# Kernel optimization log

Measured on AMD Instinct MI355X. Metric: run time of the kernel, lower is better.

## Reference

```python
import jax, jax.numpy as jnp
import numpy as np

HEADS = 8
KV_HEADS = 4
HEAD_DIM = 256
HIDDEN = 2560
WINDOW = 1024          # sliding_window (layer is sliding: (0+1) % 6 != 0)
SCALE = 256.0 ** -0.5  # query_pre_attn_scalar ** -0.5
ROPE_BASE = 10000.0    # rope_local_base_freq for sliding layers
EPS = 1e-6
NEG = -1e30


def rms_norm(x, w, eps=EPS):
    # x: [..., D]; effective weight is (1 + param) per the RMSNorm module
    var = jnp.mean(x * x, axis=-1, keepdims=True)
    return x * jax.lax.rsqrt(var + eps) * w


def rope(x, base, offset):
    # x: [B, H, T, D]; rotate-half RoPE over the full head_dim
    T, D = x.shape[2], x.shape[3]
    half = D // 2
    pos = (offset + jnp.arange(T)).astype(jnp.float32)           # [T]
    inv_freq = base ** (-jnp.arange(half, dtype=jnp.float32) * 2.0 / D)  # [half]
    ang = pos[:, None] * inv_freq[None, :]                       # [T, half]
    cos, sin = jnp.cos(ang), jnp.sin(ang)
    x1, x2 = x[..., :half], x[..., half:]
    return jnp.concatenate([x1 * cos - x2 * sin, x2 * cos + x1 * sin], axis=-1)


def setup_inputs() -> dict:
    key = jax.random.key(0)
    ks = jax.random.split(key, 7)
    B, T, S = 2, 1024, 4096
    w_std = 0.02
    return {
        "x": jax.random.normal(ks[0], (B, T, HIDDEN), dtype=jnp.float32),
        "k_cache": jax.random.normal(ks[1], (B, KV_HEADS, S, HEAD_DIM), dtype=jnp.float32),
        "v_cache": jax.random.normal(ks[2], (B, KV_HEADS, S, HEAD_DIM), dtype=jnp.float32),
        "wq": jax.random.normal(ks[3], (HIDDEN, HEADS * HEAD_DIM), dtype=jnp.float32) * w_std,
        "wk": jax.random.normal(ks[4], (HIDDEN, KV_HEADS * HEAD_DIM), dtype=jnp.float32) * w_std,
        "wv": jax.random.normal(ks[5], (HIDDEN, KV_HEADS * HEAD_DIM), dtype=jnp.float32) * w_std,
        "wo": jax.random.normal(ks[6], (HEADS * HEAD_DIM, HIDDEN), dtype=jnp.float32) * w_std,
        "q_norm_w": jnp.zeros((HEAD_DIM,), dtype=jnp.float32),
        "k_norm_w": jnp.zeros((HEAD_DIM,), dtype=jnp.float32),
        "pos_offset": 2048,
        "cache_index": 2048,
    }


def reference(x, k_cache, v_cache, wq, wk, wv, wo, q_norm_w, k_norm_w, pos_offset, cache_index):
    B, T, _ = x.shape
    # QKV projections -> [B, H, T, D]
    q = (x @ wq).reshape(B, T, HEADS, HEAD_DIM).transpose(0, 2, 1, 3)
    k = (x @ wk).reshape(B, T, KV_HEADS, HEAD_DIM).transpose(0, 2, 1, 3)
    v = (x @ wv).reshape(B, T, KV_HEADS, HEAD_DIM).transpose(0, 2, 1, 3)
    # per-head RMSNorm (effective weight 1 + param)
    q = rms_norm(q, 1.0 + q_norm_w)
    k = rms_norm(k, 1.0 + k_norm_w)
    # RoPE with position offset
    q = rope(q, ROPE_BASE, pos_offset)
    k = rope(k, ROPE_BASE, pos_offset)
    # KV cache update at cache_index along the sequence axis
    k_new = jax.lax.dynamic_update_slice(k_cache, k, (0, 0, cache_index, 0))
    v_new = jax.lax.dynamic_update_slice(v_cache, v, (0, 0, cache_index, 0))
    S = k_new.shape[2]
    # sliding-window validity mask over cached keys (as in the module: shared over queries)
    idx = jnp.arange(S)
    valid = (idx < cache_index + T) & (idx >= cache_index + T - WINDOW)   # [S]
    # GQA attention: group queries over kv heads
    G = HEADS // KV_HEADS
    qg = q.reshape(B, KV_HEADS, G, T, HEAD_DIM)
    scores = jnp.einsum('bkgtd,bksd->bkgts', qg, k_new) * SCALE           # [B,KV,G,T,S]
    scores = jnp.where(valid[None, None, None, None, :], scores, NEG)
    p = jax.nn.softmax(scores, axis=-1)
    out = jnp.einsum('bkgts,bksd->bkgtd', p, v_new)                       # [B,KV,G,T,D]
    out = out.reshape(B, HEADS, T, HEAD_DIM).transpose(0, 2, 1, 3).reshape(B, T, HEADS * HEAD_DIM)
    return out @ wo, k_new, v_new
```

## Files before the change

kernel.cpp:

```cpp
#include <hip/hip_runtime.h>

typedef __bf16 bf16;
typedef __bf16 bf16x8 __attribute__((ext_vector_type(8)));
typedef __bf16 bf16x4 __attribute__((ext_vector_type(4)));
typedef float f32x4 __attribute__((ext_vector_type(4)));

#define MFMA16(a, b, c) __builtin_amdgcn_mfma_f32_16x16x32_bf16(a, b, c, 0, 0, 0)

#define GLL(lds, g)                                                    \
  __builtin_amdgcn_global_load_lds(                                    \
      (const __attribute__((address_space(1))) void*)(g),              \
      (__attribute__((address_space(3))) void*)(lds), 16, 0, 0)

__global__ __launch_bounds__(256) void cache_copy_kernel(
    const float* __restrict__ kc, const float* __restrict__ vc,
    float* __restrict__ kout, float* __restrict__ vout,
    const int* __restrict__ p_ci) {
  const int s = blockIdx.x * 4 + (threadIdx.x >> 6);
  const int bk = blockIdx.y;
  const int ci = *p_ci;
  if ((unsigned)(s - ci) < 1024u) return;
  const long base = ((long)bk * 4096 + s) * 64 + (threadIdx.x & 63);
  ((float4*)kout)[base] = ((const float4*)kc)[base];
  ((float4*)vout)[base] = ((const float4*)vc)[base];
}

__global__ __launch_bounds__(256) void cvt_x_kernel(const float* __restrict__ x,
                                                    bf16* __restrict__ xb) {
  const long i = (long)blockIdx.x * 256 + threadIdx.x;
  const float4 v = ((const float4*)x)[i];
  bf16x4 o4;
  o4.x = (bf16)v.x; o4.y = (bf16)v.y; o4.z = (bf16)v.z; o4.w = (bf16)v.w;
  ((bf16x4*)xb)[i] = o4;
}

__global__ __launch_bounds__(256) void wqkv_trans_kernel(const float* __restrict__ wq,
                                                         const float* __restrict__ wk,
                                                         const float* __restrict__ wv,
                                                         bf16* __restrict__ dst) {
  __shared__ float tile[32][33];
  const int k0 = blockIdx.x * 32, n0 = blockIdx.y * 32;
  const float* src; int col, srcN;
  if (n0 < 2048)      { src = wq; col = n0;        srcN = 2048; }
  else if (n0 < 3072) { src = wk; col = n0 - 2048; srcN = 1024; }
  else                { src = wv; col = n0 - 3072; srcN = 1024; }
  const int tx = threadIdx.x, ty = threadIdx.y;
#pragma unroll
  for (int i = 0; i < 4; ++i)
    tile[ty + i * 8][tx] = src[(long)(k0 + ty + i * 8) * srcN + col + tx];
  __syncthreads();
#pragma unroll
  for (int i = 0; i < 4; ++i)
    dst[(long)(n0 + ty + i * 8) * 2560 + k0 + tx] = (bf16)tile[tx][ty + i * 8];
}

__global__ __launch_bounds__(256) void wo_trans_kernel(const float* __restrict__ wo,
                                                       bf16* __restrict__ dst) {
  __shared__ float tile[32][33];
  const int k0 = blockIdx.x * 32, n0 = blockIdx.y * 32;
  const int tx = threadIdx.x, ty = threadIdx.y;
#pragma unroll
  for (int i = 0; i < 4; ++i)
    tile[ty + i * 8][tx] = wo[(long)(k0 + ty + i * 8) * 2560 + n0 + tx];
  __syncthreads();
#pragma unroll
  for (int i = 0; i < 4; ++i)
    dst[(long)(n0 + ty + i * 8) * 2048 + k0 + tx] = (bf16)tile[tx][ty + i * 8];
}

__global__ __launch_bounds__(256) void v_trans_kernel(const float* __restrict__ vout,
                                                      const int* __restrict__ p_ci,
                                                      bf16* __restrict__ vt) {
  __shared__ float tile[32][33];
  const int s0 = blockIdx.x * 32, d0 = blockIdx.y * 32, bk = blockIdx.z;
  const int ci = *p_ci;
  const int tx = threadIdx.x, ty = threadIdx.y;
  const float* src = vout + ((long)bk * 4096 + ci) * 256;
#pragma unroll
  for (int i = 0; i < 4; ++i)
    tile[ty + i * 8][tx] = src[(long)(s0 + ty + i * 8) * 256 + d0 + tx];
  __syncthreads();
  bf16* dstb = vt + ((long)bk * 256 + d0) * 1024 + s0;
#pragma unroll
  for (int i = 0; i < 4; ++i)
    dstb[(long)(ty + i * 8) * 1024 + tx] = (bf16)tile[tx][ty + i * 8];
}

template <int K, int N>
__global__ __launch_bounds__(256) void gemm_kernel(const bf16* __restrict__ A,
                                                   const bf16* __restrict__ BT,
                                                   float* __restrict__ C) {
  __shared__ bf16 As[128 * 64];
  __shared__ bf16 Bs[64 * 64];
  const int bm = blockIdx.x, bn = blockIdx.y;
  const int tid = threadIdx.x;
  const int wave = tid >> 6, lane = tid & 63;
  const int quad = lane >> 4, l16 = lane & 15;
  const int wm = (wave & 1) * 64, wn = (wave >> 1) * 32;
  f32x4 acc[4][2] = {};
  const int srow = tid >> 3;
  const int scol = tid & 7;
  const bf16* Ag = A + (long)(bm * 128) * K;
  const bf16* Bg = BT + (long)(bn * 64) * K;
  for (int k0 = 0; k0 < K; k0 += 64) {
    __syncthreads();
#pragma unroll
    for (int i = 0; i < 4; ++i) {
      const int r = i * 32 + srow;
      GLL(As + (i * 256 + wave * 64) * 8, Ag + (long)r * K + k0 + (scol ^ (r & 7)) * 8);
    }
#pragma unroll
    for (int i = 0; i < 2; ++i) {
      const int r = i * 32 + srow;
      GLL(Bs + (i * 256 + wave * 64) * 8, Bg + (long)r * K + k0 + (scol ^ (r & 7)) * 8);
    }
    __syncthreads();
#pragma unroll
    for (int kk = 0; kk < 2; ++kk) {
      bf16x8 af[4], bfr[2];
#pragma unroll
      for (int mi = 0; mi < 4; ++mi) {
        const int r = wm + mi * 16 + l16;
        af[mi] = *(const bf16x8*)(As + r * 64 + (((kk * 4 + quad) ^ (r & 7)) * 8));
      }
#pragma unroll
      for (int ni = 0; ni < 2; ++ni) {
        const int r = wn + ni * 16 + l16;
        bfr[ni] = *(const bf16x8*)(Bs + r * 64 + (((kk * 4 + quad) ^ (r & 7)) * 8));
      }
#pragma unroll
      for (int mi = 0; mi < 4; ++mi)
#pragma unroll
        for (int ni = 0; ni < 2; ++ni)
          acc[mi][ni] = MFMA16(af[mi], bfr[ni], acc[mi][ni]);
    }
  }
  const int crow = bm * 128 + wm + quad * 4;
  const int ccol = bn * 64 + wn + l16;
#pragma unroll
  for (int mi = 0; mi < 4; ++mi)
#pragma unroll
    for (int ni = 0; ni < 2; ++ni)
#pragma unroll
      for (int r = 0; r < 4; ++r)
        C[(long)(crow + mi * 16 + r) * N + ccol + ni * 16] = acc[mi][ni][r];
}

__global__ __launch_bounds__(256) void normrope_kernel(
    const float* __restrict__ qkv, const float* __restrict__ qw,
    const float* __restrict__ kw, const int* __restrict__ p_pos,
    const int* __restrict__ p_ci, float* __restrict__ kout,
    float* __restrict__ vout, bf16* __restrict__ q_bf, bf16* __restrict__ k_bf) {
  const int bt = blockIdx.x, slot = blockIdx.y;
  const int t = bt & 1023, b = bt >> 10;
  const int d = threadIdx.x;
  const float val = qkv[(long)bt * 4096 + slot * 256 + d];
  const int ci = *p_ci;
  if (slot >= 12) {
    vout[((long)(b * 4 + (slot - 12)) * 4096 + ci + t) * 256 + d] = val;
    return;
  }
  __shared__ float red[4];
  __shared__ float rowbuf[256];
  float ss = val * val;
#pragma unroll
  for (int i = 1; i < 64; i <<= 1) ss += __shfl_xor(ss, i);
  if ((d & 63) == 0) red[d >> 6] = ss;
  __syncthreads();
  const float tot = red[0] + red[1] + red[2] + red[3];
  const float rstd = rsqrtf(tot * (1.0f / 256.0f) + 1e-6f);
  const bool isq = slot < 8;
  const float wv = isq ? qw[d] : kw[d];
  const float nv = val * rstd * (1.0f + wv);
  rowbuf[d] = nv;
  __syncthreads();
  const int e = d & 127;
  const float inv_freq = exp2f((float)e * -0.10381025296522976f);
  const float ang = (float)(*p_pos + t) * inv_freq;
  float sn, cs;
  sincosf(ang, &sn, &cs);
  float outv;
  if (d < 128) outv = nv * cs - rowbuf[d + 128] * sn;
  else         outv = nv * cs + rowbuf[d - 128] * sn;
  if (isq) {
    q_bf[((long)(b * 8 + slot) * 1024 + t) * 256 + d] = (bf16)outv;
  } else {
    const int kh = slot - 8;
    kout[((long)(b * 4 + kh) * 4096 + ci + t) * 256 + d] = outv;
    k_bf[((long)(b * 4 + kh) * 1024 + t) * 256 + d] = (bf16)outv;
  }
}

__global__ __launch_bounds__(256) void attn_kernel(const bf16* __restrict__ q_bf,
                                                   const bf16* __restrict__ k_bf,
                                                   const bf16* __restrict__ vt_bf,
                                                   bf16* __restrict__ attn) {
  __shared__ bf16 Ks[64 * 256];
  __shared__ bf16 Vs[256 * 64];
  __shared__ bf16 Ps[64 * 72];
  const int qt = blockIdx.x, h = blockIdx.y, b = blockIdx.z;
  const int kvh = h >> 1;
  const int tid = threadIdx.x;
  const int wave = tid >> 6, lane = tid & 63, quad = lane >> 4, l16 = lane & 15;
  bf16x8 qf[8];
  const bf16* qg =
      q_bf + ((long)(b * 8 + h) * 1024 + qt * 64 + wave * 16 + l16) * 256 + quad * 8;
#pragma unroll
  for (int i = 0; i < 8; ++i) qf[i] = *(const bf16x8*)(qg + i * 32);
  f32x4 o[16] = {};
  float m_r[4] = {-1e30f, -1e30f, -1e30f, -1e30f};
  float l_r[4] = {0.f, 0.f, 0.f, 0.f};
  const float sfac = 0.0625f * 1.44269504088896f;
  const bf16* kgb = k_bf + (long)(b * 4 + kvh) * 1024 * 256;
  const bf16* vgb = vt_bf + (long)(b * 4 + kvh) * 256 * 1024;
  const int krow = tid >> 5, kccp = tid & 31;
  const int kcc = kccp ^ (krow & 7);
  const int vrow0 = tid >> 3, vccp = tid & 7;
  for (int st = 0; st < 16; ++st) {
    __syncthreads();
#pragma unroll
    for (int i = 0; i < 8; ++i) {
      GLL(Ks + (i * 256 + wave * 64) * 8,
          kgb + (long)(st * 64 + krow + i * 8) * 256 + kcc * 8);
    }
#pragma unroll
    for (int i = 0; i < 8; ++i) {
      const int vr = vrow0 + i * 32;
      GLL(Vs + (i * 256 + wave * 64) * 8,
          vgb + (long)vr * 1024 + st * 64 + (vccp ^ (vr & 7)) * 8);
    }
    __syncthreads();
    f32x4 sacc[4] = {};
#pragma unroll
    for (int kk = 0; kk < 8; ++kk) {
#pragma unroll
      for (int ni = 0; ni < 4; ++ni) {
        const int r = ni * 16 + l16;
        bf16x8 kf = *(const bf16x8*)(Ks + r * 256 + (((kk * 4 + quad) ^ (r & 7)) * 8));
        sacc[ni] = MFMA16(qf[kk], kf, sacc[ni]);
      }
    }
    float alpha_r[4];
#pragma unroll
    for (int r = 0; r < 4; ++r) {
      float s0 = sacc[0][r] * sfac, s1 = sacc[1][r] * sfac;
      float s2 = sacc[2][r] * sfac, s3 = sacc[3][r] * sfac;
      float mx = fmaxf(fmaxf(s0, s1), fmaxf(s2, s3));
#pragma unroll
      for (int dd = 1; dd < 16; dd <<= 1) mx = fmaxf(mx, __shfl_xor(mx, dd));
      float mnew = fmaxf(m_r[r], mx);
      float al = exp2f(m_r[r] - mnew);
      m_r[r] = mnew;
      alpha_r[r] = al;
      float p0 = exp2f(s0 - mnew), p1 = exp2f(s1 - mnew);
      float p2 = exp2f(s2 - mnew), p3 = exp2f(s3 - mnew);
      float rs = p0 + p1 + p2 + p3;
#pragma unroll
      for (int dd = 1; dd < 16; dd <<= 1) rs += __shfl_xor(rs, dd);
      l_r[r] = l_r[r] * al + rs;
      const int prow = (wave * 16 + quad * 4 + r) * 72;
      Ps[prow + l16] = (bf16)p0;
      Ps[prow + 16 + l16] = (bf16)p1;
      Ps[prow + 32 + l16] = (bf16)p2;
      Ps[prow + 48 + l16] = (bf16)p3;
    }
#pragma unroll
    for (int n2 = 0; n2 < 16; ++n2) {
      f32x4 tv = o[n2];
      tv.x *= alpha_r[0]; tv.y *= alpha_r[1]; tv.z *= alpha_r[2]; tv.w *= alpha_r[3];
      o[n2] = tv;
    }
    __syncthreads();
    bf16x8 pf0 = *(const bf16x8*)(Ps + (wave * 16 + l16) * 72 + quad * 8);
    bf16x8 pf1 = *(const bf16x8*)(Ps + (wave * 16 + l16) * 72 + 32 + quad * 8);
#pragma unroll
    for (int n2 = 0; n2 < 16; ++n2) {
      const int r = n2 * 16 + l16;
      bf16x8 vf0 = *(const bf16x8*)(Vs + r * 64 + ((quad ^ (r & 7)) * 8));
      o[n2] = MFMA16(pf0, vf0, o[n2]);
      bf16x8 vf1 = *(const bf16x8*)(Vs + r * 64 + (((4 + quad) ^ (r & 7)) * 8));
      o[n2] = MFMA16(pf1, vf1, o[n2]);
    }
  }
  float inv_l[4];
#pragma unroll
  for (int r = 0; r < 4; ++r) inv_l[r] = 1.0f / l_r[r];
  bf16* og = attn + ((long)(b * 1024 + qt * 64 + wave * 16 + quad * 4)) * 2048 +
             h * 256 + l16;
#pragma unroll
  for (int n2 = 0; n2 < 16; ++n2)
#pragma unroll
    for (int r = 0; r < 4; ++r)
      og[(long)r * 2048 + n2 * 16] = (bf16)(o[n2][r] * inv_l[r]);
}

extern "C" void kernel_launch(void* const* d_in, const int* in_sizes, int n_in,
                              void* d_out, int out_size, void* d_ws, size_t ws_size,
                              hipStream_t stream) {
  const float* x = (const float*)d_in[0];
  const float* k_cache = (const float*)d_in[1];
  const float* v_cache = (const float*)d_in[2];
  const float* wq = (const float*)d_in[3];
  const float* wk = (const float*)d_in[4];
  const float* wv = (const float*)d_in[5];
  const float* wo = (const float*)d_in[6];
  const float* qnw = (const float*)d_in[7];
  const float* knw = (const float*)d_in[8];
  const int* p_pos = (const int*)d_in[9];
  const int* p_ci = (const int*)d_in[10];

  float* out0 = (float*)d_out;
  float* kout = out0 + (long)2 * 1024 * 2560;
  float* vout = kout + (long)2 * 4 * 4096 * 256;

  char* w = (char*)d_ws;
  bf16* x_bf = (bf16*)(w);
  bf16* wqkv_t = (bf16*)(w + 10485760);
  bf16* wo_t = (bf16*)(w + 31457280);
  float* qkv = (float*)(w + 41943040);
  bf16* q_bf = (bf16*)(w + 75497472);
  bf16* k_bf = (bf16*)(w + 83886080);
  bf16* vt_bf = (bf16*)(w + 88080384);
  bf16* attn_b = (bf16*)(w + 92274688);

  cache_copy_kernel<<<dim3(1024, 8), 256, 0, stream>>>(k_cache, v_cache, kout,
                                                       vout, p_ci);

  cvt_x_kernel<<<5120, 256, 0, stream>>>(x, x_bf);
  dim3 tb(32, 8);
  wqkv_trans_kernel<<<dim3(80, 128), tb, 0, stream>>>(wq, wk, wv, wqkv_t);
  wo_trans_kernel<<<dim3(64, 80), tb, 0, stream>>>(wo, wo_t);

  gemm_kernel<2560, 4096><<<dim3(16, 64), 256, 0, stream>>>(x_bf, wqkv_t, qkv);

  normrope_kernel<<<dim3(2048, 16), 256, 0, stream>>>(qkv, qnw, knw, p_pos, p_ci,
                                                      kout, vout, q_bf, k_bf);

  v_trans_kernel<<<dim3(32, 8, 8), tb, 0, stream>>>(vout, p_ci, vt_bf);

  attn_kernel<<<dim3(16, 8, 2), 256, 0, stream>>>(q_bf, k_bf, vt_bf, attn_b);

  gemm_kernel<2048, 2560><<<dim3(16, 40), 256, 0, stream>>>(attn_b, wo_t, out0);
}
```

Baseline: 395.5 us.

## Merge prep kernels, double-buffer GEMM, bf16 QKV intermediate, retune tiles

Four preprocessing kernels (cache copy, x conversion, two weight transposes) are merged into one launch that dispatches on block index. The GEMM is templated on tile sizes and now double-buffers LDS with a K-step of 32, so the next tile's global-to-LDS load overlaps the current MFMA work. The QKV projection writes a bf16 intermediate instead of fp32, which halves that traffic. Tile shapes change for both GEMMs. The bf16 intermediate adds rounding before the RMS norm and also flows into the stored V cache values.

Result: no change. 398.8 us (+0.9%).

```diff
diff --git a/kernel.cpp b/kernel.cpp
--- a/kernel.cpp
+++ b/kernel.cpp
@@ -12,60 +12,63 @@
       (const __attribute__((address_space(1))) void*)(g),              \
       (__attribute__((address_space(3))) void*)(lds), 16, 0, 0)
 
-__global__ __launch_bounds__(256) void cache_copy_kernel(
+__global__ __launch_bounds__(256) void prep_kernel(
     const float* __restrict__ kc, const float* __restrict__ vc,
     float* __restrict__ kout, float* __restrict__ vout,
-    const int* __restrict__ p_ci) {
-  const int s = blockIdx.x * 4 + (threadIdx.x >> 6);
-  const int bk = blockIdx.y;
-  const int ci = *p_ci;
-  if ((unsigned)(s - ci) < 1024u) return;
-  const long base = ((long)bk * 4096 + s) * 64 + (threadIdx.x & 63);
-  ((float4*)kout)[base] = ((const float4*)kc)[base];
-  ((float4*)vout)[base] = ((const float4*)vc)[base];
-}
-
-__global__ __launch_bounds__(256) void cvt_x_kernel(const float* __restrict__ x,
-                                                    bf16* __restrict__ xb) {
-  const long i = (long)blockIdx.x * 256 + threadIdx.x;
-  const float4 v = ((const float4*)x)[i];
-  bf16x4 o4;
-  o4.x = (bf16)v.x; o4.y = (bf16)v.y; o4.z = (bf16)v.z; o4.w = (bf16)v.w;
-  ((bf16x4*)xb)[i] = o4;
-}
-
-__global__ __launch_bounds__(256) void wqkv_trans_kernel(const float* __restrict__ wq,
-                                                         const float* __restrict__ wk,
-                                                         const float* __restrict__ wv,
-                                                         bf16* __restrict__ dst) {
+    const int* __restrict__ p_ci, const float* __restrict__ x,
+    bf16* __restrict__ xb, const float* __restrict__ wq,
+    const float* __restrict__ wk, const float* __restrict__ wv,
+    bf16* __restrict__ wqkv_t, const float* __restrict__ wo,
+    bf16* __restrict__ wo_t) {
+  const int blk = blockIdx.x;
+  const int tid = threadIdx.x;
+  if (blk < 8192) {
+    const int s = (blk & 1023) * 4 + (tid >> 6);
+    const int bk = blk >> 10;
+    const int ci = *p_ci;
+    if ((unsigned)(s - ci) < 1024u) return;
+    const long base = ((long)bk * 4096 + s) * 64 + (tid & 63);
+    ((float4*)kout)[base] = ((const float4*)kc)[base];
+    ((float4*)vout)[base] = ((const float4*)vc)[base];
+    return;
+  }
+  if (blk < 13312) {
+    const long i = (long)(blk - 8192) * 256 + tid;
+    const float4 v = ((const float4*)x)[i];
+    bf16x4 o4;
+    o4.x = (bf16)v.x; o4.y = (bf16)v.y; o4.z = (bf16)v.z; o4.w = (bf16)v.w;
+    ((bf16x4*)xb)[i] = o4;
+    return;
+  }
   __shared__ float tile[32][33];
-  const int k0 = blockIdx.x * 32, n0 = blockIdx.y * 32;
-  const float* src; int col, srcN;
-  if (n0 < 2048)      { src = wq; col = n0;        srcN = 2048; }
-  else if (n0 < 3072) { src = wk; col = n0 - 2048; srcN = 1024; }
-  else                { src = wv; col = n0 - 3072; srcN = 1024; }
-  const int tx = threadIdx.x, ty = threadIdx.y;
-#pragma unroll
-  for (int i = 0; i < 4; ++i)
-    tile[ty + i * 8][tx] = src[(long)(k0 + ty + i * 8) * srcN + col + tx];
-  __syncthreads();
-#pragma unroll
-  for (int i = 0; i < 4; ++i)
-    dst[(long)(n0 + ty + i * 8) * 2560 + k0 + tx] = (bf16)tile[tx][ty + i * 8];
-}
-
-__global__ __launch_bounds__(256) void wo_trans_kernel(const float* __restrict__ wo,
-                                                       bf16* __restrict__ dst) {
-  __shared__ float tile[32][33];
-  const int k0 = blockIdx.x * 32, n0 = blockIdx.y * 32;
-  const int tx = threadIdx.x, ty = threadIdx.y;
-#pragma unroll
-  for (int i = 0; i < 4; ++i)
-    tile[ty + i * 8][tx] = wo[(long)(k0 + ty + i * 8) * 2560 + n0 + tx];
-  __syncthreads();
-#pragma unroll
-  for (int i = 0; i < 4; ++i)
-    dst[(long)(n0 + ty + i * 8) * 2048 + k0 + tx] = (bf16)tile[tx][ty + i * 8];
+  const int tx = tid & 31, ty = tid >> 5;
+  if (blk < 23552) {
+    const int idx = blk - 13312;
+    const int k0 = (idx % 80) * 32, n0 = (idx / 80) * 32;
+    const float* src; int col, srcN;
+    if (n0 < 2048)      { src = wq; col = n0;        srcN = 2048; }
+    else if (n0 < 3072) { src = wk; col = n0 - 2048; srcN = 1024; }
+    else                { src = wv; col = n0 - 3072; srcN = 1024; }
+#pragma unroll
+    for (int i = 0; i < 4; ++i)
+      tile[ty + i * 8][tx] = src[(long)(k0 + ty + i * 8) * srcN + col + tx];
+    __syncthreads();
+#pragma unroll
+    for (int i = 0; i < 4; ++i)
+      wqkv_t[(long)(n0 + ty + i * 8) * 2560 + k0 + tx] = (bf16)tile[tx][ty + i * 8];
+    return;
+  }
+  {
+    const int idx = blk - 23552;
+    const int k0 = (idx & 63) * 32, n0 = (idx >> 6) * 32;
+#pragma unroll
+    for (int i = 0; i < 4; ++i)
+      tile[ty + i * 8][tx] = wo[(long)(k0 + ty + i * 8) * 2560 + n0 + tx];
+    __syncthreads();
+#pragma unroll
+    for (int i = 0; i < 4; ++i)
+      wo_t[(long)(n0 + ty + i * 8) * 2048 + k0 + tx] = (bf16)tile[tx][ty + i * 8];
+  }
 }
 
 __global__ __launch_bounds__(256) void v_trans_kernel(const float* __restrict__ vout,
@@ -86,75 +89,85 @@
     dstb[(long)(ty + i * 8) * 1024 + tx] = (bf16)tile[tx][ty + i * 8];
 }
 
-template <int K, int N>
+template <int BM, int BN, int K, int N, typename OutT>
 __global__ __launch_bounds__(256) void gemm_kernel(const bf16* __restrict__ A,
                                                    const bf16* __restrict__ BT,
-                                                   float* __restrict__ C) {
-  __shared__ bf16 As[128 * 64];
-  __shared__ bf16 Bs[64 * 64];
+                                                   OutT* __restrict__ C) {
+  __shared__ bf16 As[2 * BM * 32];
+  __shared__ bf16 Bs[2 * BN * 32];
   const int bm = blockIdx.x, bn = blockIdx.y;
   const int tid = threadIdx.x;
   const int wave = tid >> 6, lane = tid & 63;
   const int quad = lane >> 4, l16 = lane & 15;
-  const int wm = (wave & 1) * 64, wn = (wave >> 1) * 32;
-  f32x4 acc[4][2] = {};
-  const int srow = tid >> 3;
-  const int scol = tid & 7;
-  const bf16* Ag = A + (long)(bm * 128) * K;
-  const bf16* Bg = BT + (long)(bn * 64) * K;
-  for (int k0 = 0; k0 < K; k0 += 64) {
-    __syncthreads();
-#pragma unroll
-    for (int i = 0; i < 4; ++i) {
-      const int r = i * 32 + srow;
-      GLL(As + (i * 256 + wave * 64) * 8, Ag + (long)r * K + k0 + (scol ^ (r & 7)) * 8);
-    }
-#pragma unroll
-    for (int i = 0; i < 2; ++i) {
-      const int r = i * 32 + srow;
-      GLL(Bs + (i * 256 + wave * 64) * 8, Bg + (long)r * K + k0 + (scol ^ (r & 7)) * 8);
-    }
-    __syncthreads();
-#pragma unroll
-    for (int kk = 0; kk < 2; ++kk) {
-      bf16x8 af[4], bfr[2];
-#pragma unroll
-      for (int mi = 0; mi < 4; ++mi) {
-        const int r = wm + mi * 16 + l16;
-        af[mi] = *(const bf16x8*)(As + r * 64 + (((kk * 4 + quad) ^ (r & 7)) * 8));
-      }
-#pragma unroll
-      for (int ni = 0; ni < 2; ++ni) {
-        const int r = wn + ni * 16 + l16;
-        bfr[ni] = *(const bf16x8*)(Bs + r * 64 + (((kk * 4 + quad) ^ (r & 7)) * 8));
-      }
-#pragma unroll
-      for (int mi = 0; mi < 4; ++mi)
-#pragma unroll
-        for (int ni = 0; ni < 2; ++ni)
-          acc[mi][ni] = MFMA16(af[mi], bfr[ni], acc[mi][ni]);
-    }
-  }
-  const int crow = bm * 128 + wm + quad * 4;
-  const int ccol = bn * 64 + wn + l16;
-#pragma unroll
-  for (int mi = 0; mi < 4; ++mi)
-#pragma unroll
-    for (int ni = 0; ni < 2; ++ni)
+  constexpr int WM = BM / 2, WN = BN / 2;
+  constexpr int MI = WM / 16, NI = WN / 16;
+  const int wm = (wave & 1) * WM, wn = (wave >> 1) * WN;
+  f32x4 acc[MI][NI] = {};
+  const int srow = tid >> 2;
+  const int sslot = tid & 3;
+  const bf16* Ag = A + (long)(bm * BM) * K;
+  const bf16* Bg = BT + (long)(bn * BN) * K;
+  auto stage = [&](int buf, int k0) {
+#pragma unroll
+    for (int i = 0; i < BM / 64; ++i) {
+      const int r = i * 64 + srow;
+      const int cc = (sslot - (r >> 1)) & 3;
+      GLL(As + buf * BM * 32 + (i * 256 + wave * 64) * 8,
+          Ag + (long)r * K + k0 + cc * 8);
+    }
+#pragma unroll
+    for (int i = 0; i < BN / 64; ++i) {
+      const int r = i * 64 + srow;
+      const int cc = (sslot - (r >> 1)) & 3;
+      GLL(Bs + buf * BN * 32 + (i * 256 + wave * 64) * 8,
+          Bg + (long)r * K + k0 + cc * 8);
+    }
+  };
+  stage(0, 0);
+  int buf = 0;
+  for (int k0 = 0; k0 < K; k0 += 32) {
+    __syncthreads();
+    if (k0 + 32 < K) stage(buf ^ 1, k0 + 32);
+    const bf16* Ab = As + buf * BM * 32;
+    const bf16* Bb = Bs + buf * BN * 32;
+    bf16x8 af[MI], bfr[NI];
+#pragma unroll
+    for (int mi = 0; mi < MI; ++mi) {
+      const int r = wm + mi * 16 + l16;
+      af[mi] = *(const bf16x8*)(Ab + r * 32 + (((quad + (r >> 1)) & 3) * 8));
+    }
+#pragma unroll
+    for (int ni = 0; ni < NI; ++ni) {
+      const int r = wn + ni * 16 + l16;
+      bfr[ni] = *(const bf16x8*)(Bb + r * 32 + (((quad + (r >> 1)) & 3) * 8));
+    }
+#pragma unroll
+    for (int mi = 0; mi < MI; ++mi)
+#pragma unroll
+      for (int ni = 0; ni < NI; ++ni)
+        acc[mi][ni] = MFMA16(af[mi], bfr[ni], acc[mi][ni]);
+    buf ^= 1;
+  }
+  const int crow = bm * BM + wm + quad * 4;
+  const int ccol = bn * BN + wn + l16;
+#pragma unroll
+  for (int mi = 0; mi < MI; ++mi)
+#pragma unroll
+    for (int ni = 0; ni < NI; ++ni)
 #pragma unroll
       for (int r = 0; r < 4; ++r)
-        C[(long)(crow + mi * 16 + r) * N + ccol + ni * 16] = acc[mi][ni][r];
+        C[(long)(crow + mi * 16 + r) * N + ccol + ni * 16] = (OutT)acc[mi][ni][r];
 }
 
 __global__ __launch_bounds__(256) void normrope_kernel(
-    const float* __restrict__ qkv, const float* __restrict__ qw,
+    const bf16* __restrict__ qkv, const float* __restrict__ qw,
     const float* __restrict__ kw, const int* __restrict__ p_pos,
     const int* __restrict__ p_ci, float* __restrict__ kout,
     float* __restrict__ vout, bf16* __restrict__ q_bf, bf16* __restrict__ k_bf) {
   const int bt = blockIdx.x, slot = blockIdx.y;
   const int t = bt & 1023, b = bt >> 10;
   const int d = threadIdx.x;
-  const float val = qkv[(long)bt * 4096 + slot * 256 + d];
+  const float val = (float)qkv[(long)bt * 4096 + slot * 256 + d];
   const int ci = *p_ci;
   if (slot >= 12) {
     vout[((long)(b * 4 + (slot - 12)) * 4096 + ci + t) * 256 + d] = val;
@@ -317,28 +330,26 @@
   bf16* x_bf = (bf16*)(w);
   bf16* wqkv_t = (bf16*)(w + 10485760);
   bf16* wo_t = (bf16*)(w + 31457280);
-  float* qkv = (float*)(w + 41943040);
-  bf16* q_bf = (bf16*)(w + 75497472);
-  bf16* k_bf = (bf16*)(w + 83886080);
-  bf16* vt_bf = (bf16*)(w + 88080384);
-  bf16* attn_b = (bf16*)(w + 92274688);
-
-  cache_copy_kernel<<<dim3(1024, 8), 256, 0, stream>>>(k_cache, v_cache, kout,
-                                                       vout, p_ci);
-
-  cvt_x_kernel<<<5120, 256, 0, stream>>>(x, x_bf);
-  dim3 tb(32, 8);
-  wqkv_trans_kernel<<<dim3(80, 128), tb, 0, stream>>>(wq, wk, wv, wqkv_t);
-  wo_trans_kernel<<<dim3(64, 80), tb, 0, stream>>>(wo, wo_t);
-
-  gemm_kernel<2560, 4096><<<dim3(16, 64), 256, 0, stream>>>(x_bf, wqkv_t, qkv);
+  bf16* qkv = (bf16*)(w + 41943040);
+  bf16* q_bf = (bf16*)(w + 58720256);
+  bf16* k_bf = (bf16*)(w + 67108864);
+  bf16* vt_bf = (bf16*)(w + 71303168);
+  bf16* attn_b = (bf16*)(w + 75497472);
+
+  prep_kernel<<<28672, 256, 0, stream>>>(k_cache, v_cache, kout, vout, p_ci, x,
+                                         x_bf, wq, wk, wv, wqkv_t, wo, wo_t);
+
+  gemm_kernel<128, 128, 2560, 4096, bf16>
+      <<<dim3(16, 32), 256, 0, stream>>>(x_bf, wqkv_t, qkv);
 
   normrope_kernel<<<dim3(2048, 16), 256, 0, stream>>>(qkv, qnw, knw, p_pos, p_ci,
                                                       kout, vout, q_bf, k_bf);
 
+  dim3 tb(32, 8);
   v_trans_kernel<<<dim3(32, 8, 8), tb, 0, stream>>>(vout, p_ci, vt_bf);
 
   attn_kernel<<<dim3(16, 8, 2), 256, 0, stream>>>(q_bf, k_bf, vt_bf, attn_b);
 
-  gemm_kernel<2048, 2560><<<dim3(16, 40), 256, 0, stream>>>(attn_b, wo_t, out0);
-}
+  gemm_kernel<64, 128, 2048, 2560, float>
+      <<<dim3(32, 20), 256, 0, stream>>>(attn_b, wo_t, out0);
+}
```
